# Performance work log

Hardware: AMD Instinct MI355X
Metric: run time of the kernel (lower is better)

## Reference

```python
import jax, jax.numpy as jnp
import numpy as np

D = 1024
H = 16
DH = D // H  # 64

def setup_inputs() -> dict:
    key = jax.random.key(0)
    ks = jax.random.split(key, 9)
    B, S = 2, 2048
    s = 1.0 / np.sqrt(D)
    return {
        "embed": jax.random.normal(ks[0], (B, S, D), dtype=jnp.float32),
        "Wq": jax.random.normal(ks[1], (D, D), dtype=jnp.float32) * s,
        "Wk": jax.random.normal(ks[2], (D, D), dtype=jnp.float32) * s,
        "Wv": jax.random.normal(ks[3], (D, D), dtype=jnp.float32) * s,
        "bv": jax.random.normal(ks[4], (D,), dtype=jnp.float32) * 0.01,
        "W1": jax.random.normal(ks[5], (2 * D, D), dtype=jnp.float32) * s,
        "b1": jax.random.normal(ks[6], (2 * D,), dtype=jnp.float32) * 0.01,
        "W2": jax.random.normal(ks[7], (D, 2 * D), dtype=jnp.float32) * (1.0 / np.sqrt(2 * D)),
        "b2": jax.random.normal(ks[8], (D,), dtype=jnp.float32) * 0.01,
    }

def reference(embed, Wq, Wk, Wv, bv, W1, b1, W2, b2):
    B, S, _ = embed.shape
    # torch nn.Linear: y = x @ W.T (+ b)
    Q = embed @ Wq.T                      # [B,S,D]
    K = embed @ Wk.T                      # [B,S,D]
    V = embed @ Wv.T + bv                 # [B,S,D]
    # split heads: the per-head python loop in the original is a vmap over H
    Qh = Q.reshape(B, S, H, DH)
    Kh = K.reshape(B, S, H, DH)
    Vh = V.reshape(B, S, H, DH)
    scores = jnp.einsum('bqhd,bkhd->bhqk', Qh, Kh) / np.sqrt(DH)
    attn = jax.nn.softmax(scores, axis=-1)          # [B,H,S,S]
    out = jnp.einsum('bhqk,bkhd->bqhd', attn, Vh).reshape(B, S, D)
    # FFN (use_ffn)
    out = jax.nn.relu(out @ W1.T + b1) @ W2.T + b2
    # residual (use_residue)
    return out + embed
```

## Files before the change

kernel.cpp:

```cpp
#include <hip/hip_runtime.h>
#include <hip/hip_bf16.h>

typedef unsigned short u16;
typedef unsigned int u32;
typedef __attribute__((ext_vector_type(8))) short short8;
typedef __attribute__((ext_vector_type(4))) float f32x4;
typedef __attribute__((ext_vector_type(4))) u16 u16x4;
typedef __attribute__((ext_vector_type(4))) u32 u32x4;

__device__ __forceinline__ u16 f2bf(float f) {
  unsigned u = __builtin_bit_cast(unsigned, f);
  u = (u + 0x7FFFu + ((u >> 16) & 1u)) >> 16;
  return (u16)u;
}

__device__ __forceinline__ u32 cvt_pk_bf16(float lo, float hi) {
  u32 r;
  asm("v_cvt_pk_bf16_f32 %0, %1, %2" : "=v"(r) : "v"(lo), "v"(hi));
  return r;
}

__device__ __forceinline__ void gload16(const void* g, void* l) {
  __builtin_amdgcn_global_load_lds(
      (const __attribute__((address_space(1))) void*)g,
      (__attribute__((address_space(3))) void*)l, 16, 0, 0);
}

__global__ __launch_bounds__(256) void cvt_all(
    const float* __restrict__ e, const float* __restrict__ wq,
    const float* __restrict__ wk, const float* __restrict__ wv,
    const float* __restrict__ w1, const float* __restrict__ w2,
    u16* __restrict__ ebf, u16* __restrict__ wqkv,
    u16* __restrict__ w1b, u16* __restrict__ w2b)
{
  int i = blockIdx.x * 256 + threadIdx.x;
  const float* src;
  u16* dst;
  if (i < 1048576)       { src = e;  dst = ebf; }
  else if (i < 1310720)  { src = wq; dst = wqkv;           i -= 1048576; }
  else if (i < 1572864)  { src = wk; dst = wqkv + 1048576; i -= 1310720; }
  else if (i < 1835008)  { src = wv; dst = wqkv + 2097152; i -= 1572864; }
  else if (i < 2359296)  { src = w1; dst = w1b;            i -= 1835008; }
  else                   { src = w2; dst = w2b;            i -= 2359296; }
  const float4 v = reinterpret_cast<const float4*>(src)[i];
  u16x4 o = { f2bf(v.x), f2bf(v.y), f2bf(v.z), f2bf(v.w) };
  *reinterpret_cast<u16x4*>(dst + (size_t)i * 4) = o;
}

template<int MODE, int BM>
__global__ __launch_bounds__(256, 3) void gemm_bt(
    const u16* __restrict__ A, const u16* __restrict__ W,
    const float* __restrict__ bias, const float* __restrict__ resid,
    void* __restrict__ out0, void* __restrict__ out1, void* __restrict__ out2,
    int M, int N, int K)
{
  constexpr int II = BM / 32;
  __shared__ __align__(16) u16 At[BM * 64];
  __shared__ __align__(16) u16 Bt[128 * 64];
  const int tid = threadIdx.x, lane = tid & 63, wid = tid >> 6;
  const int g = lane >> 4, c = lane & 15;
  const int wr = (wid >> 1) * (BM / 2), wc = (wid & 1) * 64;
  const int m0 = blockIdx.y * BM, n0 = blockIdx.x * 128;
  const int lrow = lane >> 3;
  const int lch = (lane & 7) ^ lrow;
  const int rsw = c & 7;

  f32x4 acc[II][4];
  #pragma unroll
  for (int i = 0; i < II; i++)
    #pragma unroll
    for (int j = 0; j < 4; j++)
      acc[i][j] = (f32x4){0.f, 0.f, 0.f, 0.f};

  const u16* Ab = A + (size_t)m0 * K;
  const u16* Wb = W + (size_t)n0 * K;

  for (int k0 = 0; k0 < K; k0 += 64) {
    __syncthreads();
    #pragma unroll
    for (int i = 0; i < II; i++) {
      const int r0 = (wid * II + i) * 8;
      gload16(Ab + (size_t)(r0 + lrow) * K + k0 + lch * 8, &At[r0 * 64]);
    }
    #pragma unroll
    for (int i = 0; i < 4; i++) {
      const int r0 = (wid * 4 + i) * 8;
      gload16(Wb + (size_t)(r0 + lrow) * K + k0 + lch * 8, &Bt[r0 * 64]);
    }
    __syncthreads();
    #pragma unroll
    for (int kh = 0; kh < 2; kh++) {
      short8 af[II], bw[4];
      #pragma unroll
      for (int i = 0; i < II; i++)
        af[i] = *reinterpret_cast<const short8*>(
            &At[(wr + i * 16 + c) * 64 + (((g + 4 * kh) ^ rsw) * 8)]);
      #pragma unroll
      for (int j = 0; j < 4; j++)
        bw[j] = *reinterpret_cast<const short8*>(
            &Bt[(wc + j * 16 + c) * 64 + (((g + 4 * kh) ^ rsw) * 8)]);
      #pragma unroll
      for (int i = 0; i < II; i++)
        #pragma unroll
        for (int j = 0; j < 4; j++)
          acc[i][j] = __builtin_amdgcn_mfma_f32_16x16x32_bf16(af[i], bw[j], acc[i][j], 0, 0, 0);
    }
  }

  #pragma unroll
  for (int i = 0; i < II; i++) {
    #pragma unroll
    for (int j = 0; j < 4; j++) {
      const int n = n0 + wc + j * 16 + c;
      const int mb = m0 + wr + i * 16 + g * 4;
      if (MODE == 1) {
        const int seg = n >> 10, nn = n & 1023;
        const int h = nn >> 6, d = nn & 63;
        const int bb = mb >> 11, s = mb & 2047;
        if (seg == 2) {
          const float bval = bias[nn];
          u16x4 o;
          #pragma unroll
          for (int r = 0; r < 4; r++) o[r] = f2bf(acc[i][j][r] + bval);
          const int s32 = s & 31;
          const int t2 = (s & ~31) + ((s32 >> 2) & 3) * 8 + ((s32 >> 4) & 1) * 4;
          *reinterpret_cast<u16x4*>(reinterpret_cast<u16*>(out2) +
              ((size_t)((bb << 4) + h) * 64 + d) * 2048 + t2) = o;
        } else {
          u16* dst = reinterpret_cast<u16*>(seg ? out1 : out0);
          const float sc = seg ? 1.0f : 0.18033688f;
          #pragma unroll
          for (int r = 0; r < 4; r++)
            dst[((size_t)((bb << 4) + h) * 2048 + s + r) * 64 + d] = f2bf(acc[i][j][r] * sc);
        }
      } else if (MODE == 3) {
        const float bval = bias[n];
        #pragma unroll
        for (int r = 0; r < 4; r++) {
          float v = fmaxf(acc[i][j][r] + bval, 0.f);
          reinterpret_cast<u16*>(out0)[(size_t)(mb + r) * N + n] = f2bf(v);
        }
      } else {
        const float bval = bias[n];
        #pragma unroll
        for (int r = 0; r < 4; r++) {
          const int m = mb + r;
          reinterpret_cast<float*>(out0)[(size_t)m * N + n] =
              acc[i][j][r] + bval + resid[(size_t)m * N + n];
        }
      }
    }
  }
}

__global__ __launch_bounds__(256, 2) void attn_kernel(
    const u16* __restrict__ Qh, const u16* __restrict__ Kh,
    const u16* __restrict__ Vt, u16* __restrict__ ao)
{
  __shared__ __align__(16) u16 Kt[2][64 * 64];
  __shared__ __align__(16) u16 Vl[2][64 * 64];

  const int tid = threadIdx.x;
  const int lane = tid & 63, wid = tid >> 6;
  const int g = lane >> 4, c = lane & 15;
  const int bh = blockIdx.y;
  const int q0 = blockIdx.x * 128 + wid * 32;
  const int lrow = lane >> 3;
  const int lch = (lane & 7) ^ lrow;
  const int rsw = c & 7;

  short8 bq[2][2];
  #pragma unroll
  for (int qt = 0; qt < 2; qt++) {
    const u16* qrow = Qh + ((size_t)bh * 2048 + q0 + qt * 16 + c) * 64;
    bq[qt][0] = *reinterpret_cast<const short8*>(qrow + g * 8);
    bq[qt][1] = *reinterpret_cast<const short8*>(qrow + 32 + g * 8);
  }

  f32x4 acc[2][4];
  #pragma unroll
  for (int qt = 0; qt < 2; qt++)
    #pragma unroll
    for (int dt = 0; dt < 4; dt++)
      acc[qt][dt] = (f32x4){0.f, 0.f, 0.f, 0.f};
  f32x4 accl[2] = {(f32x4){0.f, 0.f, 0.f, 0.f}, (f32x4){0.f, 0.f, 0.f, 0.f}};
  const short8 ones = {0x3F80, 0x3F80, 0x3F80, 0x3F80, 0x3F80, 0x3F80, 0x3F80, 0x3F80};

  const u16* Kb = Kh + (size_t)bh * 2048 * 64;
  const u16* Vb = Vt + (size_t)bh * 64 * 2048;

  auto stage = [&](int buf, int t0) {
    #pragma unroll
    for (int i = 0; i < 2; i++) {
      const int r0 = (wid * 2 + i) * 8;
      gload16(Kb + (size_t)(t0 + r0 + lrow) * 64 + lch * 8, &Kt[buf][r0 * 64]);
    }
    #pragma unroll
    for (int i = 0; i < 2; i++) {
      const int r0 = (wid * 2 + i) * 8;
      gload16(Vb + (size_t)(r0 + lrow) * 2048 + t0 + lch * 8, &Vl[buf][r0 * 64]);
    }
  };

  stage(0, 0);

  int cur = 0;
  for (int t0 = 0; t0 < 2048; t0 += 64, cur ^= 1) {
    __syncthreads();
    if (t0 + 64 < 2048) stage(cur ^ 1, t0 + 64);

    #pragma unroll
    for (int cp = 0; cp < 2; cp++) {
      f32x4 sv[2][2];
      __builtin_amdgcn_s_setprio(1);
      #pragma unroll
      for (int h = 0; h < 2; h++) {
        const u16* kr = &Kt[cur][(cp * 32 + h * 16 + c) * 64];
        short8 ka  = *reinterpret_cast<const short8*>(kr + ((g ^ rsw) * 8));
        short8 ka2 = *reinterpret_cast<const short8*>(kr + (((g + 4) ^ rsw) * 8));
        #pragma unroll
        for (int qt = 0; qt < 2; qt++) {
          f32x4 z = (f32x4){0.f, 0.f, 0.f, 0.f};
          z = __builtin_amdgcn_mfma_f32_16x16x32_bf16(ka, bq[qt][0], z, 0, 0, 0);
          z = __builtin_amdgcn_mfma_f32_16x16x32_bf16(ka2, bq[qt][1], z, 0, 0, 0);
          sv[qt][h] = z;
        }
      }
      __builtin_amdgcn_s_setprio(0);

      short8 pk[2];
      #pragma unroll
      for (int qt = 0; qt < 2; qt++) {
        float p[8];
        #pragma unroll
        for (int i = 0; i < 8; i++)
          p[i] = __builtin_amdgcn_exp2f(sv[qt][i >> 2][i & 3]);
        u32x4 w;
        #pragma unroll
        for (int k = 0; k < 4; k++)
          w[k] = cvt_pk_bf16(p[2 * k], p[2 * k + 1]);
        pk[qt] = __builtin_bit_cast(short8, w);
      }

      __builtin_amdgcn_s_setprio(1);
      #pragma unroll
      for (int dt = 0; dt < 4; dt++) {
        const short8 vf = *reinterpret_cast<const short8*>(
            &Vl[cur][(dt * 16 + c) * 64 + (((cp * 4 + g) ^ rsw) * 8)]);
        acc[0][dt] = __builtin_amdgcn_mfma_f32_16x16x32_bf16(pk[0], vf, acc[0][dt], 0, 0, 0);
        acc[1][dt] = __builtin_amdgcn_mfma_f32_16x16x32_bf16(pk[1], vf, acc[1][dt], 0, 0, 0);
      }
      accl[0] = __builtin_amdgcn_mfma_f32_16x16x32_bf16(pk[0], ones, accl[0], 0, 0, 0);
      accl[1] = __builtin_amdgcn_mfma_f32_16x16x32_bf16(pk[1], ones, accl[1], 0, 0, 0);
      __builtin_amdgcn_s_setprio(0);
    }
  }

  u16* ob = ao + (size_t)(bh >> 4) * 2048 * 1024 + (bh & 15) * 64;
  #pragma unroll
  for (int qt = 0; qt < 2; qt++) {
    float lq[4];
    #pragma unroll
    for (int r = 0; r < 4; r++) lq[r] = 1.0f / accl[qt][r];
    #pragma unroll
    for (int dt = 0; dt < 4; dt++)
      #pragma unroll
      for (int r = 0; r < 4; r++) {
        const size_t q = q0 + qt * 16 + g * 4 + r;
        ob[q * 1024 + dt * 16 + c] = f2bf(acc[qt][dt][r] * lq[r]);
      }
  }
}

extern "C" void kernel_launch(void* const* d_in, const int* in_sizes, int n_in,
                              void* d_out, int out_size, void* d_ws, size_t ws_size,
                              hipStream_t stream) {
  const float* embed = (const float*)d_in[0];
  const float* Wq = (const float*)d_in[1];
  const float* Wk = (const float*)d_in[2];
  const float* Wv = (const float*)d_in[3];
  const float* bv = (const float*)d_in[4];
  const float* W1 = (const float*)d_in[5];
  const float* b1 = (const float*)d_in[6];
  const float* W2 = (const float*)d_in[7];
  const float* b2 = (const float*)d_in[8];

  char* ws = (char*)d_ws;
  u16* ebf  = (u16*)ws;  ws += (size_t)4096 * 1024 * 2;
  u16* wqkv = (u16*)ws;  ws += (size_t)3072 * 1024 * 2;
  u16* w1b  = (u16*)ws;  ws += (size_t)2048 * 1024 * 2;
  u16* w2b  = (u16*)ws;  ws += (size_t)1024 * 2048 * 2;
  u16* Qh   = (u16*)ws;  ws += (size_t)4096 * 1024 * 2;
  u16* Kh   = (u16*)ws;  ws += (size_t)4096 * 1024 * 2;
  u16* Vt   = (u16*)ws;  ws += (size_t)4096 * 1024 * 2;
  u16* ao   = (u16*)ws;  ws += (size_t)4096 * 1024 * 2;
  u16* h1   = (u16*)ws;  ws += (size_t)4096 * 2048 * 2;

  dim3 blk(256);
  cvt_all<<<dim3(11264), blk, 0, stream>>>(embed, Wq, Wk, Wv, W1, W2,
                                           ebf, wqkv, w1b, w2b);
  gemm_bt<1, 128><<<dim3(24, 32), blk, 0, stream>>>(
      ebf, wqkv, bv, nullptr, Qh, Kh, Vt, 4096, 3072, 1024);
  attn_kernel<<<dim3(16, 32), blk, 0, stream>>>(Qh, Kh, Vt, ao);
  gemm_bt<3, 128><<<dim3(16, 32), blk, 0, stream>>>(
      ao, w1b, b1, nullptr, h1, nullptr, nullptr, 4096, 2048, 1024);
  gemm_bt<4, 64><<<dim3(8, 64), blk, 0, stream>>>(
      h1, w2b, b2, embed, d_out, nullptr, nullptr, 4096, 1024, 2048);
}
```

Baseline: 144.3 us.

## Split attention key range in two and merge partials in a combine kernel

Result: no change. 145.3 us (+0.7%).

```diff
diff --git a/kernel.cpp b/kernel.cpp
--- a/kernel.cpp
+++ b/kernel.cpp
@@ -153,9 +153,10 @@
   }
 }
 
-__global__ __launch_bounds__(256, 2) void attn_kernel(
+__global__ __launch_bounds__(256, 4) void attn_kernel(
     const u16* __restrict__ Qh, const u16* __restrict__ Kh,
-    const u16* __restrict__ Vt, u16* __restrict__ ao)
+    const u16* __restrict__ Vt, u16* __restrict__ apart,
+    float* __restrict__ lpart)
 {
   __shared__ __align__(16) u16 Kt[2][64 * 64];
   __shared__ __align__(16) u16 Vl[2][64 * 64];
@@ -163,8 +164,13 @@
   const int tid = threadIdx.x;
   const int lane = tid & 63, wid = tid >> 6;
   const int g = lane >> 4, c = lane & 15;
-  const int bh = blockIdx.y;
-  const int q0 = blockIdx.x * 128 + wid * 32;
+
+  const int v = (blockIdx.x & 7) * 128 + (blockIdx.x >> 3);
+  const int half = v >> 9, rem = v & 511;
+  const int bh = rem >> 4, xq = rem & 15;
+  const int q0 = xq * 128 + wid * 32;
+  const int tbase = half * 1024;
+
   const int lrow = lane >> 3;
   const int lch = (lane & 7) ^ lrow;
   const int rsw = c & 7;
@@ -202,12 +208,12 @@
     }
   };
 
-  stage(0, 0);
+  stage(0, tbase);
 
   int cur = 0;
-  for (int t0 = 0; t0 < 2048; t0 += 64, cur ^= 1) {
+  for (int t0 = tbase; t0 < tbase + 1024; t0 += 64, cur ^= 1) {
     __syncthreads();
-    if (t0 + 64 < 2048) stage(cur ^ 1, t0 + 64);
+    if (t0 + 64 < tbase + 1024) stage(cur ^ 1, t0 + 64);
 
     #pragma unroll
     for (int cp = 0; cp < 2; cp++) {
@@ -256,20 +262,47 @@
     }
   }
 
-  u16* ob = ao + (size_t)(bh >> 4) * 2048 * 1024 + (bh & 15) * 64;
+  u16* ob = apart + ((size_t)(half * 32 + bh) * 2048) * 64;
   #pragma unroll
   for (int qt = 0; qt < 2; qt++) {
-    float lq[4];
-    #pragma unroll
-    for (int r = 0; r < 4; r++) lq[r] = 1.0f / accl[qt][r];
     #pragma unroll
     for (int dt = 0; dt < 4; dt++)
       #pragma unroll
       for (int r = 0; r < 4; r++) {
         const size_t q = q0 + qt * 16 + g * 4 + r;
-        ob[q * 1024 + dt * 16 + c] = f2bf(acc[qt][dt][r] * lq[r]);
-      }
-  }
+        ob[q * 64 + dt * 16 + c] = f2bf(acc[qt][dt][r]);
+      }
+    if (c == 0) {
+      #pragma unroll
+      for (int r = 0; r < 4; r++)
+        lpart[(size_t)(half * 32 + bh) * 2048 + q0 + qt * 16 + g * 4 + r] = accl[qt][r];
+    }
+  }
+}
+
+__global__ __launch_bounds__(256) void attn_combine(
+    const u16* __restrict__ apart, const float* __restrict__ lpart,
+    u16* __restrict__ ao)
+{
+  const int idx = blockIdx.x * 256 + threadIdx.x;
+  const int d4 = idx & 15;
+  const int q = (idx >> 4) & 2047;
+  const int bh = idx >> 15;
+  const size_t p0 = ((size_t)bh * 2048 + q) * 64 + d4 * 4;
+  const size_t p1 = ((size_t)(32 + bh) * 2048 + q) * 64 + d4 * 4;
+  u16x4 a0 = *reinterpret_cast<const u16x4*>(apart + p0);
+  u16x4 a1 = *reinterpret_cast<const u16x4*>(apart + p1);
+  const float l = lpart[(size_t)bh * 2048 + q] + lpart[(size_t)(32 + bh) * 2048 + q];
+  const float inv = 1.0f / l;
+  u16x4 o;
+  #pragma unroll
+  for (int i = 0; i < 4; i++) {
+    const float f0 = __builtin_bit_cast(float, (u32)a0[i] << 16);
+    const float f1 = __builtin_bit_cast(float, (u32)a1[i] << 16);
+    o[i] = f2bf((f0 + f1) * inv);
+  }
+  *reinterpret_cast<u16x4*>(
+      ao + ((size_t)(bh >> 4) * 2048 + q) * 1024 + (bh & 15) * 64 + d4 * 4) = o;
 }
 
 extern "C" void kernel_launch(void* const* d_in, const int* in_sizes, int n_in,
@@ -296,12 +329,16 @@
   u16* ao   = (u16*)ws;  ws += (size_t)4096 * 1024 * 2;
   u16* h1   = (u16*)ws;  ws += (size_t)4096 * 2048 * 2;
 
+  u16* apart = h1;
+  float* lpart = (float*)ebf;
+
   dim3 blk(256);
   cvt_all<<<dim3(11264), blk, 0, stream>>>(embed, Wq, Wk, Wv, W1, W2,
                                            ebf, wqkv, w1b, w2b);
   gemm_bt<1, 128><<<dim3(24, 32), blk, 0, stream>>>(
       ebf, wqkv, bv, nullptr, Qh, Kh, Vt, 4096, 3072, 1024);
-  attn_kernel<<<dim3(16, 32), blk, 0, stream>>>(Qh, Kh, Vt, ao);
+  attn_kernel<<<dim3(1024), blk, 0, stream>>>(Qh, Kh, Vt, apart, lpart);
+  attn_combine<<<dim3(4096), blk, 0, stream>>>(apart, lpart, ao);
   gemm_bt<3, 128><<<dim3(16, 32), blk, 0, stream>>>(
       ao, w1b, b1, nullptr, h1, nullptr, nullptr, 4096, 2048, 1024);
   gemm_bt<4, 64><<<dim3(8, 64), blk, 0, stream>>>(
```

## Split attention key range across two wave teams with LDS reduction

Applied to the files above, without the earlier changes.

Result: no change. 146.3 us (+1.4%).

```diff
diff --git a/kernel.cpp b/kernel.cpp
--- a/kernel.cpp
+++ b/kernel.cpp
@@ -153,18 +153,25 @@
   }
 }
 
-__global__ __launch_bounds__(256, 2) void attn_kernel(
+__global__ __launch_bounds__(512, 4) void attn_kernel(
     const u16* __restrict__ Qh, const u16* __restrict__ Kh,
     const u16* __restrict__ Vt, u16* __restrict__ ao)
 {
-  __shared__ __align__(16) u16 Kt[2][64 * 64];
-  __shared__ __align__(16) u16 Vl[2][64 * 64];
+  __shared__ __align__(16) u16 smem[32768];
 
   const int tid = threadIdx.x;
   const int lane = tid & 63, wid = tid >> 6;
+  const int team = wid >> 2, qw = wid & 3;
   const int g = lane >> 4, c = lane & 15;
-  const int bh = blockIdx.y;
-  const int q0 = blockIdx.x * 128 + wid * 32;
+
+  const int v = (blockIdx.x & 7) * 64 + (blockIdx.x >> 3);
+  const int bh = v >> 4, xq = v & 15;
+  const int q0 = xq * 128 + qw * 32;
+  const int tbase = team * 1024;
+
+  u16* Ktb[2] = { smem + team * 8192, smem + team * 8192 + 4096 };
+  u16* Vlb[2] = { smem + 16384 + team * 8192, smem + 16384 + team * 8192 + 4096 };
+
   const int lrow = lane >> 3;
   const int lch = (lane & 7) ^ lrow;
   const int rsw = c & 7;
@@ -192,22 +199,18 @@
   auto stage = [&](int buf, int t0) {
     #pragma unroll
     for (int i = 0; i < 2; i++) {
-      const int r0 = (wid * 2 + i) * 8;
-      gload16(Kb + (size_t)(t0 + r0 + lrow) * 64 + lch * 8, &Kt[buf][r0 * 64]);
-    }
-    #pragma unroll
-    for (int i = 0; i < 2; i++) {
-      const int r0 = (wid * 2 + i) * 8;
-      gload16(Vb + (size_t)(r0 + lrow) * 2048 + t0 + lch * 8, &Vl[buf][r0 * 64]);
+      const int r0 = (qw * 2 + i) * 8;
+      gload16(Kb + (size_t)(t0 + r0 + lrow) * 64 + lch * 8, Ktb[buf] + r0 * 64);
+      gload16(Vb + (size_t)(r0 + lrow) * 2048 + t0 + lch * 8, Vlb[buf] + r0 * 64);
     }
   };
 
-  stage(0, 0);
+  stage(0, tbase);
 
   int cur = 0;
-  for (int t0 = 0; t0 < 2048; t0 += 64, cur ^= 1) {
+  for (int t0 = tbase; t0 < tbase + 1024; t0 += 64, cur ^= 1) {
     __syncthreads();
-    if (t0 + 64 < 2048) stage(cur ^ 1, t0 + 64);
+    if (t0 + 64 < tbase + 1024) stage(cur ^ 1, t0 + 64);
 
     #pragma unroll
     for (int cp = 0; cp < 2; cp++) {
@@ -215,7 +218,7 @@
       __builtin_amdgcn_s_setprio(1);
       #pragma unroll
       for (int h = 0; h < 2; h++) {
-        const u16* kr = &Kt[cur][(cp * 32 + h * 16 + c) * 64];
+        const u16* kr = Ktb[cur] + (cp * 32 + h * 16 + c) * 64;
         short8 ka  = *reinterpret_cast<const short8*>(kr + ((g ^ rsw) * 8));
         short8 ka2 = *reinterpret_cast<const short8*>(kr + (((g + 4) ^ rsw) * 8));
         #pragma unroll
@@ -246,7 +249,7 @@
       #pragma unroll
       for (int dt = 0; dt < 4; dt++) {
         const short8 vf = *reinterpret_cast<const short8*>(
-            &Vl[cur][(dt * 16 + c) * 64 + (((cp * 4 + g) ^ rsw) * 8)]);
+            Vlb[cur] + (dt * 16 + c) * 64 + (((cp * 4 + g) ^ rsw) * 8));
         acc[0][dt] = __builtin_amdgcn_mfma_f32_16x16x32_bf16(pk[0], vf, acc[0][dt], 0, 0, 0);
         acc[1][dt] = __builtin_amdgcn_mfma_f32_16x16x32_bf16(pk[1], vf, acc[1][dt], 0, 0, 0);
       }
@@ -256,19 +259,45 @@
     }
   }
 
-  u16* ob = ao + (size_t)(bh >> 4) * 2048 * 1024 + (bh & 15) * 64;
-  #pragma unroll
-  for (int qt = 0; qt < 2; qt++) {
-    float lq[4];
-    #pragma unroll
-    for (int r = 0; r < 4; r++) lq[r] = 1.0f / accl[qt][r];
-    #pragma unroll
-    for (int dt = 0; dt < 4; dt++)
-      #pragma unroll
-      for (int r = 0; r < 4; r++) {
-        const size_t q = q0 + qt * 16 + g * 4 + r;
-        ob[q * 1024 + dt * 16 + c] = f2bf(acc[qt][dt][r] * lq[r]);
-      }
+  __syncthreads();
+  float* pbuf = (float*)smem;
+  float* lbuf = (float*)smem + 128 * 68;
+
+  if (team == 1) {
+    #pragma unroll
+    for (int qt = 0; qt < 2; qt++) {
+      const int pqb = qw * 32 + qt * 16 + g * 4;
+      #pragma unroll
+      for (int dt = 0; dt < 4; dt++)
+        #pragma unroll
+        for (int r = 0; r < 4; r++)
+          pbuf[(pqb + r) * 68 + dt * 16 + c] = acc[qt][dt][r];
+      if (c == 0) {
+        #pragma unroll
+        for (int r = 0; r < 4; r++)
+          lbuf[pqb + r] = accl[qt][r];
+      }
+    }
+  }
+  __syncthreads();
+  if (team == 0) {
+    u16* ob = ao + (size_t)(bh >> 4) * 2048 * 1024 + (bh & 15) * 64;
+    #pragma unroll
+    for (int qt = 0; qt < 2; qt++) {
+      const int pqb = qw * 32 + qt * 16 + g * 4;
+      float lq[4];
+      #pragma unroll
+      for (int r = 0; r < 4; r++)
+        lq[r] = 1.0f / (accl[qt][r] + lbuf[pqb + r]);
+      #pragma unroll
+      for (int dt = 0; dt < 4; dt++)
+        #pragma unroll
+        for (int r = 0; r < 4; r++) {
+          const float o = acc[qt][dt][r] + pbuf[(pqb + r) * 68 + dt * 16 + c];
+          const size_t q = q0 + qt * 16 + g * 4 + r;
+          ob[q * 1024 + dt * 16 + c] = f2bf(o * lq[r]);
+        }
+    }
   }
 }
 
@@ -301,7 +330,7 @@
                                            ebf, wqkv, w1b, w2b);
   gemm_bt<1, 128><<<dim3(24, 32), blk, 0, stream>>>(
       ebf, wqkv, bv, nullptr, Qh, Kh, Vt, 4096, 3072, 1024);
-  attn_kernel<<<dim3(16, 32), blk, 0, stream>>>(Qh, Kh, Vt, ao);
+  attn_kernel<<<dim3(512), dim3(512), 0, stream>>>(Qh, Kh, Vt, ao);
   gemm_bt<3, 128><<<dim3(16, 32), blk, 0, stream>>>(
       ao, w1b, b1, nullptr, h1, nullptr, nullptr, 4096, 2048, 1024);
   gemm_bt<4, 64><<<dim3(8, 64), blk, 0, stream>>>(
```

## Add 256x256-tile 8-wave pipelined GEMM kernel for QKV projection

Applied to the files above, without the earlier changes.

Result: slower. 151.2 us (+4.8%).

```diff
diff --git a/kernel.cpp b/kernel.cpp
--- a/kernel.cpp
+++ b/kernel.cpp
@@ -25,6 +25,9 @@
       (const __attribute__((address_space(1))) void*)g,
       (__attribute__((address_space(3))) void*)l, 16, 0, 0);
 }
+
+#define BARR() asm volatile("s_barrier" ::: "memory")
+#define VMW(N) asm volatile("s_waitcnt vmcnt(" #N ")" ::: "memory")
 
 __global__ __launch_bounds__(256) void cvt_all(
     const float* __restrict__ e, const float* __restrict__ wq,
@@ -47,12 +50,173 @@
   *reinterpret_cast<u16x4*>(dst + (size_t)i * 4) = o;
 }
 
+__global__ __launch_bounds__(512, 2) void gemm_qkv8(
+    const u16* __restrict__ A, const u16* __restrict__ W,
+    const float* __restrict__ bias,
+    void* __restrict__ out0, void* __restrict__ out1, void* __restrict__ out2)
+{
+  constexpr int K = 1024, NT = 16;
+  __shared__ __align__(16) u16 smem[65536];
+
+  const int tid = threadIdx.x, lane = tid & 63, w = tid >> 6;
+  const int g = lane >> 4, c = lane & 15;
+  const int lrow = lane >> 3;
+  const int lch = (lane & 7) ^ lrow;
+  const int rsw = c & 7;
+  const int m0 = blockIdx.y * 256, n0 = blockIdx.x * 256;
+  const int wr2 = (w >> 2) * 64;
+  const int wcb = (w & 3) * 32;
+
+  u16* const ab0 = smem;
+  u16* const bb0 = smem + 16384;
+
+#define ABASE(bb) (smem + (bb) * 32768)
+#define BBASE(bb) (smem + (bb) * 32768 + 16384)
+
+#define STAGE_A(bb, tt, mh)                                                   \
+  {                                                                           \
+    _Pragma("unroll")                                                         \
+    for (int k = 0; k < 2; k++) {                                             \
+      const u16* s_ = A + (size_t)(m0 + (mh) * 64 + k * 128 + w * 8 + lrow) * K \
+                      + (tt) * 64 + lch * 8;                                  \
+      gload16(s_, ABASE(bb) + (mh) * 8192 + k * 4096 + w * 512);              \
+    }                                                                         \
+  }
+#define STAGE_B(bb, tt, nh)                                                   \
+  {                                                                           \
+    _Pragma("unroll")                                                         \
+    for (int k = 0; k < 2; k++) {                                             \
+      const u16* s_ = W + (size_t)(n0 + k * 128 + (w >> 2) * 64 + (nh) * 32   \
+                                   + (w & 3) * 8 + lrow) * K                  \
+                      + (tt) * 64 + lch * 8;                                  \
+      gload16(s_, BBASE(bb) + (nh) * 8192 + k * 4096 + w * 512);              \
+    }                                                                         \
+  }
+
+  f32x4 acc[8][4];
+  #pragma unroll
+  for (int i = 0; i < 8; i++)
+    #pragma unroll
+    for (int j = 0; j < 4; j++)
+      acc[i][j] = (f32x4){0.f, 0.f, 0.f, 0.f};
+
+  STAGE_A(0, 0, 0);
+  STAGE_B(0, 0, 0);
+  STAGE_B(0, 0, 1);
+  STAGE_A(0, 0, 1);
+  STAGE_A(1, 1, 0);
+  STAGE_B(1, 1, 0);
+  STAGE_B(1, 1, 1);
+
+  short8 ar[2][4][2];
+  short8 br[2][2][2];
+
+#define LDA(mh)                                                               \
+  {                                                                           \
+    _Pragma("unroll")                                                         \
+    for (int i = 0; i < 4; i++)                                               \
+      _Pragma("unroll")                                                       \
+      for (int kh = 0; kh < 2; kh++)                                          \
+        ar[mh][i][kh] = *reinterpret_cast<const short8*>(                     \
+            ABASE(b) + (mh) * 8192 + (wr2 + i * 16 + c) * 64                  \
+            + (((g + 4 * kh) ^ rsw) * 8));                                    \
+  }
+#define LDB_ALL()                                                             \
+  {                                                                           \
+    _Pragma("unroll")                                                         \
+    for (int nh = 0; nh < 2; nh++)                                            \
+      _Pragma("unroll")                                                       \
+      for (int j = 0; j < 2; j++)                                             \
+        _Pragma("unroll")                                                     \
+        for (int kh = 0; kh < 2; kh++)                                        \
+          br[nh][j][kh] = *reinterpret_cast<const short8*>(                   \
+              BBASE(b) + nh * 8192 + (wcb + j * 16 + c) * 64                  \
+              + (((g + 4 * kh) ^ rsw) * 8));                                  \
+  }
+#define QUAD(mh, nh)                                                          \
+  {                                                                           \
+    __builtin_amdgcn_s_setprio(1);                                            \
+    _Pragma("unroll")                                                         \
+    for (int i = 0; i < 4; i++)                                               \
+      _Pragma("unroll")                                                       \
+      for (int j = 0; j < 2; j++)                                             \
+        _Pragma("unroll")                                                     \
+        for (int kh = 0; kh < 2; kh++)                                        \
+          acc[(mh) * 4 + i][(nh) * 2 + j] =                                   \
+              __builtin_amdgcn_mfma_f32_16x16x32_bf16(                        \
+                  ar[mh][i][kh], br[nh][j][kh],                               \
+                  acc[(mh) * 4 + i][(nh) * 2 + j], 0, 0, 0);                  \
+    __builtin_amdgcn_s_setprio(0);                                            \
+  }
+
+  for (int t = 0; t < NT; ++t) {
+    const int b = t & 1;
+    if (t < NT - 1) { VMW(8); } else { VMW(2); }
+    BARR();
+    LDA(0);
+    LDB_ALL();
+    if (t + 1 < NT) STAGE_A(1 - b, t + 1, 1);
+    BARR();
+    QUAD(0, 0);
+    if (t < NT - 1) { VMW(8); } else { VMW(0); }
+    BARR();
+    LDA(1);
+    if (t + 2 < NT) STAGE_A(b, t + 2, 0);
+    BARR();
+    QUAD(1, 0);
+    BARR();
+    if (t + 2 < NT) STAGE_B(b, t + 2, 0);
+    BARR();
+    QUAD(0, 1);
+    BARR();
+    if (t + 2 < NT) STAGE_B(b, t + 2, 1);
+    BARR();
+    QUAD(1, 1);
+  }
+
+  const int wrE = (w >> 2) * 128, wcE = (w & 3) * 64;
+  #pragma unroll
+  for (int i = 0; i < 8; i++) {
+    #pragma unroll
+    for (int j = 0; j < 4; j++) {
+      const int n = n0 + wcE + j * 16 + c;
+      const int mb = m0 + wrE + i * 16 + g * 4;
+      const int seg = n >> 10, nn = n & 1023;
+      const int h = nn >> 6, d = nn & 63;
+      const int bb2 = mb >> 11, s = mb & 2047;
+      if (seg == 2) {
+        const float bval = bias[nn];
+        u16x4 o;
+        #pragma unroll
+        for (int r = 0; r < 4; r++) o[r] = f2bf(acc[i][j][r] + bval);
+        const int s32 = s & 31;
+        const int t2 = (s & ~31) + ((s32 >> 2) & 3) * 8 + ((s32 >> 4) & 1) * 4;
+        *reinterpret_cast<u16x4*>(reinterpret_cast<u16*>(out2) +
+            ((size_t)((bb2 << 4) + h) * 64 + d) * 2048 + t2) = o;
+      } else {
+        u16* dst = reinterpret_cast<u16*>(seg ? out1 : out0);
+        const float sc = seg ? 1.0f : 0.18033688f;
+        #pragma unroll
+        for (int r = 0; r < 4; r++)
+          dst[((size_t)((bb2 << 4) + h) * 2048 + s + r) * 64 + d] =
+              f2bf(acc[i][j][r] * sc);
+      }
+    }
+  }
+#undef ABASE
+#undef BBASE
+#undef STAGE_A
+#undef STAGE_B
+#undef LDA
+#undef LDB_ALL
+#undef QUAD
+}
+
 template<int MODE, int BM>
 __global__ __launch_bounds__(256, 3) void gemm_bt(
     const u16* __restrict__ A, const u16* __restrict__ W,
     const float* __restrict__ bias, const float* __restrict__ resid,
-    void* __restrict__ out0, void* __restrict__ out1, void* __restrict__ out2,
-    int M, int N, int K)
+    void* __restrict__ out0, int M, int N, int K)
 {
   constexpr int II = BM / 32;
   __shared__ __align__(16) u16 At[BM * 64];
@@ -113,35 +277,14 @@
     for (int j = 0; j < 4; j++) {
       const int n = n0 + wc + j * 16 + c;
       const int mb = m0 + wr + i * 16 + g * 4;
-      if (MODE == 1) {
-        const int seg = n >> 10, nn = n & 1023;
-        const int h = nn >> 6, d = nn & 63;
-        const int bb = mb >> 11, s = mb & 2047;
-        if (seg == 2) {
-          const float bval = bias[nn];
-          u16x4 o;
-          #pragma unroll
-          for (int r = 0; r < 4; r++) o[r] = f2bf(acc[i][j][r] + bval);
-          const int s32 = s & 31;
-          const int t2 = (s & ~31) + ((s32 >> 2) & 3) * 8 + ((s32 >> 4) & 1) * 4;
-          *reinterpret_cast<u16x4*>(reinterpret_cast<u16*>(out2) +
-              ((size_t)((bb << 4) + h) * 64 + d) * 2048 + t2) = o;
-        } else {
-          u16* dst = reinterpret_cast<u16*>(seg ? out1 : out0);
-          const float sc = seg ? 1.0f : 0.18033688f;
-          #pragma unroll
-          for (int r = 0; r < 4; r++)
-            dst[((size_t)((bb << 4) + h) * 2048 + s + r) * 64 + d] = f2bf(acc[i][j][r] * sc);
-        }
-      } else if (MODE == 3) {
-        const float bval = bias[n];
+      const float bval = bias[n];
+      if (MODE == 3) {
         #pragma unroll
         for (int r = 0; r < 4; r++) {
           float v = fmaxf(acc[i][j][r] + bval, 0.f);
           reinterpret_cast<u16*>(out0)[(size_t)(mb + r) * N + n] = f2bf(v);
         }
       } else {
-        const float bval = bias[n];
         #pragma unroll
         for (int r = 0; r < 4; r++) {
           const int m = mb + r;
@@ -299,11 +442,11 @@
   dim3 blk(256);
   cvt_all<<<dim3(11264), blk, 0, stream>>>(embed, Wq, Wk, Wv, W1, W2,
                                            ebf, wqkv, w1b, w2b);
-  gemm_bt<1, 128><<<dim3(24, 32), blk, 0, stream>>>(
-      ebf, wqkv, bv, nullptr, Qh, Kh, Vt, 4096, 3072, 1024);
+  gemm_qkv8<<<dim3(12, 16), dim3(512), 0, stream>>>(
+      ebf, wqkv, bv, Qh, Kh, Vt);
   attn_kernel<<<dim3(16, 32), blk, 0, stream>>>(Qh, Kh, Vt, ao);
   gemm_bt<3, 128><<<dim3(16, 32), blk, 0, stream>>>(
-      ao, w1b, b1, nullptr, h1, nullptr, nullptr, 4096, 2048, 1024);
+      ao, w1b, b1, nullptr, h1, 4096, 2048, 1024);
   gemm_bt<4, 64><<<dim3(8, 64), blk, 0, stream>>>(
-      h1, w2b, b2, embed, d_out, nullptr, nullptr, 4096, 1024, 2048);
-}
+      h1, w2b, b2, embed, d_out, 4096, 1024, 2048);
+}
```
